# Performance work log

Measured on AMD Instinct MI355X. Metric: run time of the kernel, lower is better.

Reference implementation:

```python
import jax, jax.numpy as jnp
import numpy as np

NUM_CARDS = 71
NUM_SLOTS = 71
TRUMP_DIM = 7
HIDDEN = [512, 256, 128]
ACTIONS = 9
BATCH = 16384


def setup_inputs() -> dict:
    key = jax.random.key(0)
    ks = jax.random.split(key, 16)
    state_idx = jax.random.randint(ks[0], (BATCH, NUM_SLOTS), 0, NUM_CARDS, dtype=jnp.int32)
    trump_onehot = jax.random.uniform(ks[1], (BATCH, TRUMP_DIM), dtype=jnp.float32)
    legal_mask = jnp.ones((BATCH, ACTIONS), dtype=bool)
    in_dim = NUM_SLOTS * NUM_CARDS + TRUMP_DIM  # 5048
    dims = [in_dim] + HIDDEN
    params = {}
    for i, (d_in, d_out) in enumerate(zip(dims[:-1], dims[1:])):
        params[f"W{i}"] = jax.random.normal(ks[2 + 2 * i], (d_in, d_out), dtype=jnp.float32) * 0.02
        params[f"b{i}"] = jnp.zeros((d_out,), dtype=jnp.float32)
    params["Wp"] = jax.random.normal(ks[10], (dims[-1], ACTIONS), dtype=jnp.float32) * 0.02
    params["bp"] = jnp.zeros((ACTIONS,), dtype=jnp.float32)
    return {"state_idx": state_idx, "trump_onehot": trump_onehot, "legal_mask": legal_mask, **params}


def reference(state_idx, trump_onehot, legal_mask,
              W0, b0, W1, b1, W2, b2, Wp, bp):
    # one-hot encode 71 card slots and flatten: (B, 71*71)
    idx = jnp.clip(state_idx, 0, NUM_CARDS - 1)
    one_hot = jax.nn.one_hot(idx, NUM_CARDS, dtype=jnp.float32)
    flat = one_hot.reshape(one_hot.shape[0], -1)
    x = jnp.concatenate([flat, trump_onehot], axis=1)  # (B, 5048)
    x = jax.nn.relu(x @ W0 + b0)
    x = jax.nn.relu(x @ W1 + b1)
    x = jax.nn.relu(x @ W2 + b2)
    logits = x @ Wp + bp  # (B, 9)
    logits = jnp.where(legal_mask, logits, -jnp.inf)
    return jax.nn.log_softmax(logits, axis=1)
```

## Files before the change

kernel.cpp:

```cpp
#include <hip/hip_runtime.h>
#include <hip/hip_bf16.h>

typedef unsigned int u32;
typedef unsigned short u16;
typedef unsigned char u8;
typedef __attribute__((ext_vector_type(4))) float f32x4;
typedef __attribute__((ext_vector_type(8))) short short8;

#define NSLOT   71
#define NCARD   71
#define ONEHOT  5041
#define INDIM   5048
#define D0      512
#define D1      256
#define D2      128
#define NACT    9

__device__ __forceinline__ float bflo(u32 u) { u32 v = u << 16; float f; __builtin_memcpy(&f, &v, 4); return f; }
__device__ __forceinline__ float bfhi(u32 u) { u32 v = u & 0xFFFF0000u; float f; __builtin_memcpy(&f, &v, 4); return f; }
__device__ __forceinline__ u16 f2bf(float x) {
    u32 u; __builtin_memcpy(&u, &x, 4);
    u32 r = u + 0x7FFFu + ((u >> 16) & 1u);
    return (u16)(r >> 16);
}
__device__ __forceinline__ void unpack16(uint4 a, uint4 b, float* w) {
    w[0]=bflo(a.x);  w[1]=bfhi(a.x);  w[2]=bflo(a.y);  w[3]=bfhi(a.y);
    w[4]=bflo(a.z);  w[5]=bfhi(a.z);  w[6]=bflo(a.w);  w[7]=bfhi(a.w);
    w[8]=bflo(b.x);  w[9]=bfhi(b.x);  w[10]=bflo(b.y); w[11]=bfhi(b.y);
    w[12]=bflo(b.z); w[13]=bfhi(b.z); w[14]=bflo(b.w); w[15]=bfhi(b.w);
}

__global__ void prep_kernel(const float* __restrict__ W0, const float* __restrict__ W1,
                            const float* __restrict__ W2,
                            u16* __restrict__ W0bf, u16* __restrict__ W1T, u16* __restrict__ W2T) {
    int i = blockIdx.x * 256 + threadIdx.x;
    const int n0 = INDIM * D0;
    const int n1 = D0 * D1;
    const int n2 = D1 * D2;
    if (i < n0) {
        W0bf[i] = f2bf(W0[i]);
    } else if (i < n0 + n1) {
        int j = i - n0; int n = j >> 9, k = j & 511;
        W1T[j] = f2bf(W1[k * D1 + n]);
    } else if (i < n0 + n1 + n2) {
        int j = i - n0 - n1; int n = j >> 8, k = j & 255;
        W2T[j] = f2bf(W2[k * D2 + n]);
    }
}

__global__ __launch_bounds__(512)
void layer0_kernel(const int* __restrict__ sidx, const float* __restrict__ trump,
                   const float* __restrict__ b0, const u16* __restrict__ W0bf,
                   u16* __restrict__ h0) {
    __shared__ u8 idxl[256 * NSLOT];
    __shared__ float trl[256 * 7];
    const int tid = threadIdx.x;
    const int ct = blockIdx.x & 3;
    const int chunk = blockIdx.x >> 2;
    const int rbase = chunk * 256;

    for (int i = tid; i < 256 * NSLOT; i += 512) {
        int v = sidx[rbase * NSLOT + i];
        v = v < 0 ? 0 : (v > NCARD - 1 ? NCARD - 1 : v);
        idxl[i] = (u8)v;
    }
    for (int i = tid; i < 256 * 7; i += 512)
        trl[i] = trump[rbase * 7 + i];
    __syncthreads();

    const int rg = tid >> 3;
    const int cg = tid & 7;
    const int c0 = ct * 128 + cg * 16;

    float acc[4][16];
    {
        float bias[16];
        #pragma unroll
        for (int j = 0; j < 16; ++j) bias[j] = b0[c0 + j];
        #pragma unroll
        for (int i = 0; i < 4; ++i)
            #pragma unroll
            for (int j = 0; j < 16; ++j) acc[i][j] = bias[j];
        #pragma unroll
        for (int t = 0; t < 7; ++t) {
            const uint4* wp = (const uint4*)(W0bf + (size_t)(ONEHOT + t) * D0 + c0);
            uint4 wa = wp[0], wb = wp[1];
            float wv[16]; unpack16(wa, wb, wv);
            #pragma unroll
            for (int i = 0; i < 4; ++i) {
                float tv = trl[(rg * 4 + i) * 7 + t];
                #pragma unroll
                for (int j = 0; j < 16; ++j) acc[i][j] += tv * wv[j];
            }
        }
    }

    for (int s = 0; s < NSLOT; ++s) {
        const u16* base = W0bf + (size_t)s * NCARD * D0 + c0;
        #pragma unroll
        for (int i = 0; i < 4; ++i) {
            int card = idxl[(rg * 4 + i) * NSLOT + s];
            const uint4* wp = (const uint4*)(base + ((u32)card << 9));
            uint4 wa = wp[0], wb = wp[1];
            float wv[16]; unpack16(wa, wb, wv);
            #pragma unroll
            for (int j = 0; j < 16; ++j) acc[i][j] += wv[j];
        }
    }

    #pragma unroll
    for (int i = 0; i < 4; ++i) {
        int row = rbase + rg * 4 + i;
        u32 o[8];
        #pragma unroll
        for (int k = 0; k < 8; ++k) {
            u32 l16 = f2bf(fmaxf(acc[i][2 * k], 0.f));
            u32 h16 = f2bf(fmaxf(acc[i][2 * k + 1], 0.f));
            o[k] = l16 | (h16 << 16);
        }
        uint4* dst = (uint4*)(h0 + (size_t)row * D0 + c0);
        dst[0] = make_uint4(o[0], o[1], o[2], o[3]);
        dst[1] = make_uint4(o[4], o[5], o[6], o[7]);
    }
}

__global__ __launch_bounds__(512)
void mlp_kernel(const u16* __restrict__ h0, const u16* __restrict__ W1T, const u16* __restrict__ W2T,
                const float* __restrict__ b1, const float* __restrict__ b2,
                const float* __restrict__ Wp, const float* __restrict__ bp,
                const int* __restrict__ legal, float* __restrict__ out) {
    __shared__ u16 Abuf[32 * 520];
    __shared__ u16 h1buf[32 * 264];
    __shared__ u16 h2buf[32 * 136];
    __shared__ float wpb[D2 * NACT + NACT];
    const int tid = threadIdx.x;
    const int r0 = blockIdx.x * 32;

    for (int i = tid; i < 2048; i += 512) {
        int r = i >> 6, g = i & 63;
        uint4 v = *(const uint4*)(h0 + (size_t)(r0 + r) * D0 + g * 8);
        *(uint4*)&Abuf[r * 520 + g * 8] = v;
    }
    for (int i = tid; i < D2 * NACT + NACT; i += 512)
        wpb[i] = (i < D2 * NACT) ? Wp[i] : bp[i - D2 * NACT];
    __syncthreads();

    const int w  = tid >> 6;
    const int l  = tid & 63;
    const int lc = l & 15;
    const int kg = l >> 4;

    {
        const int n0 = w * 32;
        f32x4 a00 = {0.f,0.f,0.f,0.f}, a01 = a00, a10 = a00, a11 = a00;
        for (int kb = 0; kb < D0; kb += 32) {
            short8 av0 = *(const short8*)&Abuf[lc * 520 + kb + kg * 8];
            short8 av1 = *(const short8*)&Abuf[(lc + 16) * 520 + kb + kg * 8];
            short8 bv0 = *(const short8*)(W1T + (size_t)(n0 + lc) * D0 + kb + kg * 8);
            short8 bv1 = *(const short8*)(W1T + (size_t)(n0 + 16 + lc) * D0 + kb + kg * 8);
            a00 = __builtin_amdgcn_mfma_f32_16x16x32_bf16(av0, bv0, a00, 0, 0, 0);
            a01 = __builtin_amdgcn_mfma_f32_16x16x32_bf16(av0, bv1, a01, 0, 0, 0);
            a10 = __builtin_amdgcn_mfma_f32_16x16x32_bf16(av1, bv0, a10, 0, 0, 0);
            a11 = __builtin_amdgcn_mfma_f32_16x16x32_bf16(av1, bv1, a11, 0, 0, 0);
        }
        #pragma unroll
        for (int nb = 0; nb < 2; ++nb) {
            int col = n0 + nb * 16 + lc;
            float bias = b1[col];
            #pragma unroll
            for (int j = 0; j < 4; ++j) {
                f32x4 v0 = nb ? a01 : a00;
                f32x4 v1 = nb ? a11 : a10;
                h1buf[(kg * 4 + j) * 264 + col]        = f2bf(fmaxf(v0[j] + bias, 0.f));
                h1buf[(16 + kg * 4 + j) * 264 + col]   = f2bf(fmaxf(v1[j] + bias, 0.f));
            }
        }
    }
    __syncthreads();

    {
        const int n0 = w * 16;
        f32x4 c0 = {0.f,0.f,0.f,0.f}, c1 = c0;
        for (int kb = 0; kb < D1; kb += 32) {
            short8 av0 = *(const short8*)&h1buf[lc * 264 + kb + kg * 8];
            short8 av1 = *(const short8*)&h1buf[(lc + 16) * 264 + kb + kg * 8];
            short8 bv  = *(const short8*)(W2T + (size_t)(n0 + lc) * D1 + kb + kg * 8);
            c0 = __builtin_amdgcn_mfma_f32_16x16x32_bf16(av0, bv, c0, 0, 0, 0);
            c1 = __builtin_amdgcn_mfma_f32_16x16x32_bf16(av1, bv, c1, 0, 0, 0);
        }
        int col = n0 + lc;
        float bias = b2[col];
        #pragma unroll
        for (int j = 0; j < 4; ++j) {
            h2buf[(kg * 4 + j) * 136 + col]      = f2bf(fmaxf(c0[j] + bias, 0.f));
            h2buf[(16 + kg * 4 + j) * 136 + col] = f2bf(fmaxf(c1[j] + bias, 0.f));
        }
    }
    __syncthreads();

    if (tid < 128) {
        int r = tid >> 2, q = tid & 3;
        float part[NACT];
        #pragma unroll
        for (int a = 0; a < NACT; ++a) part[a] = 0.f;
        int kbase = q * 32;
        #pragma unroll
        for (int kk = 0; kk < 32; kk += 2) {
            u32 pr = *(const u32*)&h2buf[r * 136 + kbase + kk];
            float x0 = bflo(pr), x1 = bfhi(pr);
            #pragma unroll
            for (int a = 0; a < NACT; ++a)
                part[a] += x0 * wpb[(kbase + kk) * NACT + a] + x1 * wpb[(kbase + kk + 1) * NACT + a];
        }
        #pragma unroll
        for (int a = 0; a < NACT; ++a) {
            part[a] += __shfl_xor(part[a], 1, 64);
            part[a] += __shfl_xor(part[a], 2, 64);
        }
        if (q == 0) {
            int row = r0 + r;
            const int* mk = legal + (size_t)row * NACT;
            float lg[NACT]; float mx = -INFINITY;
            #pragma unroll
            for (int a = 0; a < NACT; ++a) {
                lg[a] = part[a] + wpb[D2 * NACT + a];
                if (mk[a] != 0 && lg[a] > mx) mx = lg[a];
            }
            float s = 0.f;
            #pragma unroll
            for (int a = 0; a < NACT; ++a) if (mk[a] != 0) s += __expf(lg[a] - mx);
            float lse = mx + __logf(s);
            #pragma unroll
            for (int a = 0; a < NACT; ++a)
                out[(size_t)row * NACT + a] = (mk[a] != 0) ? (lg[a] - lse) : -INFINITY;
        }
    }
}

extern "C" void kernel_launch(void* const* d_in, const int* in_sizes, int n_in,
                              void* d_out, int out_size, void* d_ws, size_t ws_size,
                              hipStream_t stream) {
    const int*   sidx  = (const int*)d_in[0];
    const float* trump = (const float*)d_in[1];
    const int*   legal = (const int*)d_in[2];
    const float* W0 = (const float*)d_in[3];
    const float* b0 = (const float*)d_in[4];
    const float* W1 = (const float*)d_in[5];
    const float* b1 = (const float*)d_in[6];
    const float* W2 = (const float*)d_in[7];
    const float* b2 = (const float*)d_in[8];
    const float* Wp = (const float*)d_in[9];
    const float* bp = (const float*)d_in[10];
    float* out = (float*)d_out;

    u16* W0bf = (u16*)d_ws;
    u16* W1T  = W0bf + (size_t)INDIM * D0;
    u16* W2T  = W1T + (size_t)D0 * D1;
    u16* h0   = W2T + (size_t)D1 * D2;

    const int total = INDIM * D0 + D0 * D1 + D1 * D2;
    prep_kernel<<<(total + 255) / 256, 256, 0, stream>>>(W0, W1, W2, W0bf, W1T, W2T);
    layer0_kernel<<<256, 512, 0, stream>>>(sidx, trump, b0, W0bf, h0);
    mlp_kernel<<<512, 512, 0, stream>>>(h0, W1T, W2T, b1, b2, Wp, bp, legal, out);
}
```

Baseline: 87.52 us.

## Switch weights and activations to fp16 with packed half accumulation in layer0

Stores weights and hidden activations as fp16 instead of bf16. Layer0 now accumulates directly in packed f16x16 vectors, which drops the bf16 unpack to fp32 and allows packed half adds, and the MLP uses fp16 MFMA. It also remaps the block index so that blocks sharing a column tile are adjacent, and adds a 64KB dummy LDS array to limit occupancy to one block per CU. Accumulating 72 terms in fp16 costs precision and carries a risk of rounding error or overflow.

```diff
diff --git a/kernel.cpp b/kernel.cpp
--- a/kernel.cpp
+++ b/kernel.cpp
@@ -4,8 +4,11 @@
 typedef unsigned int u32;
 typedef unsigned short u16;
 typedef unsigned char u8;
+typedef _Float16 f16;
+typedef __attribute__((ext_vector_type(2)))  _Float16 f16x2;
+typedef __attribute__((ext_vector_type(8)))  _Float16 f16x8;
+typedef __attribute__((ext_vector_type(16))) _Float16 f16x16;
 typedef __attribute__((ext_vector_type(4))) float f32x4;
-typedef __attribute__((ext_vector_type(8))) short short8;
 
 #define NSLOT   71
 #define NCARD   71
@@ -16,48 +19,41 @@
 #define D2      128
 #define NACT    9
 
-__device__ __forceinline__ float bflo(u32 u) { u32 v = u << 16; float f; __builtin_memcpy(&f, &v, 4); return f; }
-__device__ __forceinline__ float bfhi(u32 u) { u32 v = u & 0xFFFF0000u; float f; __builtin_memcpy(&f, &v, 4); return f; }
-__device__ __forceinline__ u16 f2bf(float x) {
-    u32 u; __builtin_memcpy(&u, &x, 4);
-    u32 r = u + 0x7FFFu + ((u >> 16) & 1u);
-    return (u16)(r >> 16);
-}
-__device__ __forceinline__ void unpack16(uint4 a, uint4 b, float* w) {
-    w[0]=bflo(a.x);  w[1]=bfhi(a.x);  w[2]=bflo(a.y);  w[3]=bfhi(a.y);
-    w[4]=bflo(a.z);  w[5]=bfhi(a.z);  w[6]=bflo(a.w);  w[7]=bfhi(a.w);
-    w[8]=bflo(b.x);  w[9]=bfhi(b.x);  w[10]=bflo(b.y); w[11]=bfhi(b.y);
-    w[12]=bflo(b.z); w[13]=bfhi(b.z); w[14]=bflo(b.w); w[15]=bfhi(b.w);
-}
+__device__ __forceinline__ u16 f2h_bits(float x) { f16 h = (f16)x; u16 r; __builtin_memcpy(&r, &h, 2); return r; }
 
 __global__ void prep_kernel(const float* __restrict__ W0, const float* __restrict__ W1,
                             const float* __restrict__ W2,
-                            u16* __restrict__ W0bf, u16* __restrict__ W1T, u16* __restrict__ W2T) {
+                            u16* __restrict__ W0h, u16* __restrict__ W1T, u16* __restrict__ W2T) {
     int i = blockIdx.x * 256 + threadIdx.x;
     const int n0 = INDIM * D0;
     const int n1 = D0 * D1;
     const int n2 = D1 * D2;
     if (i < n0) {
-        W0bf[i] = f2bf(W0[i]);
+        W0h[i] = f2h_bits(W0[i]);
     } else if (i < n0 + n1) {
         int j = i - n0; int n = j >> 9, k = j & 511;
-        W1T[j] = f2bf(W1[k * D1 + n]);
+        W1T[j] = f2h_bits(W1[k * D1 + n]);
     } else if (i < n0 + n1 + n2) {
         int j = i - n0 - n1; int n = j >> 8, k = j & 255;
-        W2T[j] = f2bf(W2[k * D2 + n]);
+        W2T[j] = f2h_bits(W2[k * D2 + n]);
     }
 }
 
 __global__ __launch_bounds__(512)
 void layer0_kernel(const int* __restrict__ sidx, const float* __restrict__ trump,
-                   const float* __restrict__ b0, const u16* __restrict__ W0bf,
+                   const float* __restrict__ b0, const u16* __restrict__ W0h,
                    u16* __restrict__ h0) {
     __shared__ u8 idxl[256 * NSLOT];
     __shared__ float trl[256 * 7];
+    __shared__ u8 ldspad[65536];
     const int tid = threadIdx.x;
-    const int ct = blockIdx.x & 3;
-    const int chunk = blockIdx.x >> 2;
+    const int ct = blockIdx.x >> 6;
+    const int chunk = blockIdx.x & 63;
     const int rbase = chunk * 256;
+
+    if (sidx[0] == 0x7fffffff) {
+        ldspad[tid] = 1; __syncthreads(); h0[tid] = ldspad[tid ^ 1];
+    }
 
     for (int i = tid; i < 256 * NSLOT; i += 512) {
         int v = sidx[rbase * NSLOT + i];
@@ -72,55 +68,40 @@
     const int cg = tid & 7;
     const int c0 = ct * 128 + cg * 16;
 
-    float acc[4][16];
+    f16x16 acc[4];
     {
-        float bias[16];
-        #pragma unroll
-        for (int j = 0; j < 16; ++j) bias[j] = b0[c0 + j];
-        #pragma unroll
-        for (int i = 0; i < 4; ++i)
-            #pragma unroll
-            for (int j = 0; j < 16; ++j) acc[i][j] = bias[j];
+        f16x16 bias;
+        #pragma unroll
+        for (int j = 0; j < 16; ++j) bias[j] = (f16)b0[c0 + j];
+        #pragma unroll
+        for (int i = 0; i < 4; ++i) acc[i] = bias;
         #pragma unroll
         for (int t = 0; t < 7; ++t) {
-            const uint4* wp = (const uint4*)(W0bf + (size_t)(ONEHOT + t) * D0 + c0);
-            uint4 wa = wp[0], wb = wp[1];
-            float wv[16]; unpack16(wa, wb, wv);
-            #pragma unroll
-            for (int i = 0; i < 4; ++i) {
-                float tv = trl[(rg * 4 + i) * 7 + t];
-                #pragma unroll
-                for (int j = 0; j < 16; ++j) acc[i][j] += tv * wv[j];
-            }
+            f16x16 wv = *(const f16x16*)(W0h + (size_t)(ONEHOT + t) * D0 + c0);
+            #pragma unroll
+            for (int i = 0; i < 4; ++i)
+                acc[i] += wv * (f16)trl[(rg * 4 + i) * 7 + t];
         }
     }
 
     for (int s = 0; s < NSLOT; ++s) {
-        const u16* base = W0bf + (size_t)s * NCARD * D0 + c0;
+        const u16* base = W0h + (size_t)s * NCARD * D0 + c0;
         #pragma unroll
         for (int i = 0; i < 4; ++i) {
             int card = idxl[(rg * 4 + i) * NSLOT + s];
-            const uint4* wp = (const uint4*)(base + ((u32)card << 9));
-            uint4 wa = wp[0], wb = wp[1];
-            float wv[16]; unpack16(wa, wb, wv);
-            #pragma unroll
-            for (int j = 0; j < 16; ++j) acc[i][j] += wv[j];
-        }
-    }
-
+            f16x16 wv = *(const f16x16*)(base + ((u32)card << 9));
+            acc[i] += wv;
+        }
+    }
+
+    const f16x16 zero = {};
     #pragma unroll
     for (int i = 0; i < 4; ++i) {
         int row = rbase + rg * 4 + i;
-        u32 o[8];
-        #pragma unroll
-        for (int k = 0; k < 8; ++k) {
-            u32 l16 = f2bf(fmaxf(acc[i][2 * k], 0.f));
-            u32 h16 = f2bf(fmaxf(acc[i][2 * k + 1], 0.f));
-            o[k] = l16 | (h16 << 16);
-        }
+        f16x16 v = __builtin_elementwise_max(acc[i], zero);
         uint4* dst = (uint4*)(h0 + (size_t)row * D0 + c0);
-        dst[0] = make_uint4(o[0], o[1], o[2], o[3]);
-        dst[1] = make_uint4(o[4], o[5], o[6], o[7]);
+        dst[0] = ((const uint4*)&v)[0];
+        dst[1] = ((const uint4*)&v)[1];
     }
 }
 
@@ -154,14 +135,14 @@
         const int n0 = w * 32;
         f32x4 a00 = {0.f,0.f,0.f,0.f}, a01 = a00, a10 = a00, a11 = a00;
         for (int kb = 0; kb < D0; kb += 32) {
-            short8 av0 = *(const short8*)&Abuf[lc * 520 + kb + kg * 8];
-            short8 av1 = *(const short8*)&Abuf[(lc + 16) * 520 + kb + kg * 8];
-            short8 bv0 = *(const short8*)(W1T + (size_t)(n0 + lc) * D0 + kb + kg * 8);
-            short8 bv1 = *(const short8*)(W1T + (size_t)(n0 + 16 + lc) * D0 + kb + kg * 8);
-            a00 = __builtin_amdgcn_mfma_f32_16x16x32_bf16(av0, bv0, a00, 0, 0, 0);
-            a01 = __builtin_amdgcn_mfma_f32_16x16x32_bf16(av0, bv1, a01, 0, 0, 0);
-            a10 = __builtin_amdgcn_mfma_f32_16x16x32_bf16(av1, bv0, a10, 0, 0, 0);
-            a11 = __builtin_amdgcn_mfma_f32_16x16x32_bf16(av1, bv1, a11, 0, 0, 0);
+            f16x8 av0 = *(const f16x8*)&Abuf[lc * 520 + kb + kg * 8];
+            f16x8 av1 = *(const f16x8*)&Abuf[(lc + 16) * 520 + kb + kg * 8];
+            f16x8 bv0 = *(const f16x8*)(W1T + (size_t)(n0 + lc) * D0 + kb + kg * 8);
+            f16x8 bv1 = *(const f16x8*)(W1T + (size_t)(n0 + 16 + lc) * D0 + kb + kg * 8);
+            a00 = __builtin_amdgcn_mfma_f32_16x16x32_f16(av0, bv0, a00, 0, 0, 0);
+            a01 = __builtin_amdgcn_mfma_f32_16x16x32_f16(av0, bv1, a01, 0, 0, 0);
+            a10 = __builtin_amdgcn_mfma_f32_16x16x32_f16(av1, bv0, a10, 0, 0, 0);
+            a11 = __builtin_amdgcn_mfma_f32_16x16x32_f16(av1, bv1, a11, 0, 0, 0);
         }
         #pragma unroll
         for (int nb = 0; nb < 2; ++nb) {
@@ -171,8 +152,8 @@
             for (int j = 0; j < 4; ++j) {
                 f32x4 v0 = nb ? a01 : a00;
                 f32x4 v1 = nb ? a11 : a10;
-                h1buf[(kg * 4 + j) * 264 + col]        = f2bf(fmaxf(v0[j] + bias, 0.f));
-                h1buf[(16 + kg * 4 + j) * 264 + col]   = f2bf(fmaxf(v1[j] + bias, 0.f));
+                h1buf[(kg * 4 + j) * 264 + col]        = f2h_bits(fmaxf(v0[j] + bias, 0.f));
+                h1buf[(16 + kg * 4 + j) * 264 + col]   = f2h_bits(fmaxf(v1[j] + bias, 0.f));
             }
         }
     }
@@ -182,18 +163,18 @@
         const int n0 = w * 16;
         f32x4 c0 = {0.f,0.f,0.f,0.f}, c1 = c0;
         for (int kb = 0; kb < D1; kb += 32) {
-            short8 av0 = *(const short8*)&h1buf[lc * 264 + kb + kg * 8];
-            short8 av1 = *(const short8*)&h1buf[(lc + 16) * 264 + kb + kg * 8];
-            short8 bv  = *(const short8*)(W2T + (size_t)(n0 + lc) * D1 + kb + kg * 8);
-            c0 = __builtin_amdgcn_mfma_f32_16x16x32_bf16(av0, bv, c0, 0, 0, 0);
-            c1 = __builtin_amdgcn_mfma_f32_16x16x32_bf16(av1, bv, c1, 0, 0, 0);
+            f16x8 av0 = *(const f16x8*)&h1buf[lc * 264 + kb + kg * 8];
+            f16x8 av1 = *(const f16x8*)&h1buf[(lc + 16) * 264 + kb + kg * 8];
+            f16x8 bv  = *(const f16x8*)(W2T + (size_t)(n0 + lc) * D1 + kb + kg * 8);
+            c0 = __builtin_amdgcn_mfma_f32_16x16x32_f16(av0, bv, c0, 0, 0, 0);
+            c1 = __builtin_amdgcn_mfma_f32_16x16x32_f16(av1, bv, c1, 0, 0, 0);
         }
         int col = n0 + lc;
         float bias = b2[col];
         #pragma unroll
         for (int j = 0; j < 4; ++j) {
-            h2buf[(kg * 4 + j) * 136 + col]      = f2bf(fmaxf(c0[j] + bias, 0.f));
-            h2buf[(16 + kg * 4 + j) * 136 + col] = f2bf(fmaxf(c1[j] + bias, 0.f));
+            h2buf[(kg * 4 + j) * 136 + col]      = f2h_bits(fmaxf(c0[j] + bias, 0.f));
+            h2buf[(16 + kg * 4 + j) * 136 + col] = f2h_bits(fmaxf(c1[j] + bias, 0.f));
         }
     }
     __syncthreads();
@@ -207,7 +188,8 @@
         #pragma unroll
         for (int kk = 0; kk < 32; kk += 2) {
             u32 pr = *(const u32*)&h2buf[r * 136 + kbase + kk];
-            float x0 = bflo(pr), x1 = bfhi(pr);
+            f16x2 hp; __builtin_memcpy(&hp, &pr, 4);
+            float x0 = (float)hp.x, x1 = (float)hp.y;
             #pragma unroll
             for (int a = 0; a < NACT; ++a)
                 part[a] += x0 * wpb[(kbase + kk) * NACT + a] + x1 * wpb[(kbase + kk + 1) * NACT + a];
@@ -253,13 +235,13 @@
     const float* bp = (const float*)d_in[10];
     float* out = (float*)d_out;
 
-    u16* W0bf = (u16*)d_ws;
-    u16* W1T  = W0bf + (size_t)INDIM * D0;
+    u16* W0h  = (u16*)d_ws;
+    u16* W1T  = W0h + (size_t)INDIM * D0;
     u16* W2T  = W1T + (size_t)D0 * D1;
     u16* h0   = W2T + (size_t)D1 * D2;
 
     const int total = INDIM * D0 + D0 * D1 + D1 * D2;
-    prep_kernel<<<(total + 255) / 256, 256, 0, stream>>>(W0, W1, W2, W0bf, W1T, W2T);
-    layer0_kernel<<<256, 512, 0, stream>>>(sidx, trump, b0, W0bf, h0);
+    prep_kernel<<<(total + 255) / 256, 256, 0, stream>>>(W0, W1, W2, W0h, W1T, W2T);
+    layer0_kernel<<<256, 512, 0, stream>>>(sidx, trump, b0, W0h, h0);
     mlp_kernel<<<512, 512, 0, stream>>>(h0, W1T, W2T, b1, b2, Wp, bp, legal, out);
 }
```

After: 100.0 us. 1.14x slower.
